# Kernel optimization log

Hardware: AMD Instinct MI355X
Metric: run time of the kernel (lower is better)

Reference implementation:

```python
import jax, jax.numpy as jnp
import numpy as np

N = 50000
F_IN = 512
H = 256
L = 52
E = 1600000


def gcn_conv(x, W, b, src, dst):
    """PyG GCNConv: add self-loops, symmetric norm D^-1/2 (A+I) D^-1/2, then X W + b.
    src/dst already include self-loops."""
    h = x @ W  # [N, H]
    deg = jax.ops.segment_sum(jnp.ones_like(dst, dtype=h.dtype), dst, num_segments=N)
    dinv = jnp.where(deg > 0, jax.lax.rsqrt(deg), 0.0)
    w = dinv[src] * dinv[dst]  # [E+N]
    out = jax.ops.segment_sum(h[src] * w[:, None], dst, num_segments=N)
    return out + b


def _branch(x, src, dst, params):
    (W1, b1), (W2, b2), (W3, b3), (We, be) = params
    x = jax.nn.relu(gcn_conv(x, W1, b1, src, dst))
    x = jax.nn.relu(gcn_conv(x, W2, b2, src, dst))
    x = jax.nn.relu(gcn_conv(x, W3, b3, src, dst))
    return gcn_conv(x, We, be, src, dst)


def setup_inputs() -> dict:
    key = jax.random.key(0)
    ks = jax.random.split(key, 32)
    d = {}
    d["x_1"] = jax.random.normal(ks[0], (N, F_IN), dtype=jnp.float32)
    d["x_2"] = jax.random.normal(ks[1], (N, F_IN), dtype=jnp.float32)
    d["edge_index_1"] = jax.random.randint(ks[2], (2, E), 0, N, dtype=jnp.int32)
    d["edge_index_2"] = jax.random.randint(ks[3], (2, E), 0, N, dtype=jnp.int32)

    def lin(k, fi, fo):
        s = 1.0 / np.sqrt(fi)
        return jax.random.uniform(k, (fi, fo), jnp.float32, -s, s)

    i = 4
    for br in (1, 2):
        fis = [F_IN, H, H, H]
        for li, nm in enumerate(["1", "2", "3", "e"]):
            d[f"Wc{nm}{br}"] = lin(ks[i], fis[li], H); i += 1
            d[f"bc{nm}{br}"] = jnp.zeros((H,), jnp.float32)
    d["w1_W"] = lin(ks[i], H, 1); i += 1
    d["w1_b"] = jnp.zeros((1,), jnp.float32)
    d["w2_W"] = lin(ks[i], H, 1); i += 1
    d["w2_b"] = jnp.zeros((1,), jnp.float32)
    d["fin_W"] = lin(ks[i], H, H); i += 1
    d["fin_b"] = jnp.zeros((H,), jnp.float32)
    d["out_W"] = lin(ks[i], H, L); i += 1
    d["out_b"] = jnp.zeros((L,), jnp.float32)
    return d


def reference(x_1, edge_index_1, x_2, edge_index_2,
              Wc11, bc11, Wc21, bc21, Wc31, bc31, Wce1, bce1,
              Wc12, bc12, Wc22, bc22, Wc32, bc32, Wce2, bce2,
              w1_W, w1_b, w2_W, w2_b, fin_W, fin_b, out_W, out_b):
    loop = jnp.arange(N)
    s1 = jnp.concatenate([edge_index_1[0], loop])
    d1 = jnp.concatenate([edge_index_1[1], loop])
    s2 = jnp.concatenate([edge_index_2[0], loop])
    d2 = jnp.concatenate([edge_index_2[1], loop])

    h1 = _branch(x_1, s1, d1, [(Wc11, bc11), (Wc21, bc21), (Wc31, bc31), (Wce1, bce1)])
    h2 = _branch(x_2, s2, d2, [(Wc12, bc12), (Wc22, bc22), (Wc32, bc32), (Wce2, bce2)])

    f1 = jax.nn.sigmoid(h1 @ w1_W + w1_b)  # [N,1]
    f2 = jax.nn.sigmoid(h2 @ w2_W + w2_b)
    f1 = f1 / (f1 + f2)
    out = f1 * h1 + (1.0 - f1) * h2
    out = jax.nn.relu(out @ fin_W + fin_b)
    return jax.nn.sigmoid(out @ out_W + out_b)
```

## Files before the change

### kernel.cpp

```cpp
#include <hip/hip_runtime.h>
#include <math.h>

#define N_NODES 50000
#define F_IN    512
#define HDIM    256
#define L_OUT   52
#define E_EDGES 1600000
#define NB1     391
#define EB      2048
#define NBLK    782

typedef short short8 __attribute__((ext_vector_type(8)));
typedef unsigned short u16x8 __attribute__((ext_vector_type(8)));
typedef float f32x4 __attribute__((ext_vector_type(4)));
typedef float f32x2 __attribute__((ext_vector_type(2)));

__device__ __forceinline__ float bf2f(unsigned short u) {
    unsigned int x = ((unsigned int)u) << 16;
    return __builtin_bit_cast(float, x);
}
__device__ __forceinline__ unsigned short f2bf(float f) {
    unsigned int u = __builtin_bit_cast(unsigned int, f);
    return (unsigned short)((u + 0x7fffu + ((u >> 16) & 1u)) >> 16);
}
__device__ __forceinline__ unsigned char f2fp8(float f) {
    int pk = __builtin_amdgcn_cvt_pk_fp8_f32(f, 0.f, 0, false);
    return (unsigned char)(pk & 0xff);
}
__device__ __forceinline__ void gload16(const unsigned short* g, unsigned short* l) {
    __builtin_amdgcn_global_load_lds(
        (const __attribute__((address_space(1))) unsigned int*)(g),
        (__attribute__((address_space(3))) unsigned int*)(l), 16, 0, 0);
}


__global__ __launch_bounds__(256) void k_hist(const int* __restrict__ d1, const int* __restrict__ d2,
                                              int* __restrict__ h1, int* __restrict__ h2, int E) {
    const int* D = blockIdx.y ? d2 : d1;
    int* H = blockIdx.y ? h2 : h1;
    __shared__ int h[NB1];
    for (int t = threadIdx.x; t < NB1; t += 256) h[t] = 0;
    __syncthreads();
    int base = blockIdx.x * EB;
#pragma unroll
    for (int k = 0; k < 8; k++) {
        int e = base + k * 256 + threadIdx.x;
        if (e < E) atomicAdd(&h[D[e] >> 7], 1);
    }
    __syncthreads();
    for (int t = threadIdx.x; t < NB1; t += 256)
        H[(size_t)t * NBLK + blockIdx.x] = h[t];
}

__global__ __launch_bounds__(256) void k_scanb(int* __restrict__ h1, int* __restrict__ h2,
                                               int* __restrict__ t1, int* __restrict__ t2) {
    int* H = blockIdx.y ? h2 : h1;
    int* T = blockIdx.y ? t2 : t1;
    int b = blockIdx.x;
    __shared__ int s[256];
    int carry = 0;
    for (int base = 0; base < NBLK; base += 256) {
        int i = base + threadIdx.x;
        int v = (i < NBLK) ? H[(size_t)b * NBLK + i] : 0;
        s[threadIdx.x] = v;
        __syncthreads();
        for (int off = 1; off < 256; off <<= 1) {
            int t = (threadIdx.x >= off) ? s[threadIdx.x - off] : 0;
            __syncthreads();
            s[threadIdx.x] += t;
            __syncthreads();
        }
        if (i < NBLK) H[(size_t)b * NBLK + i] = carry + s[threadIdx.x] - v;
        int ct = s[255];
        __syncthreads();
        carry += ct;
    }
    if (threadIdx.x == 0) T[b] = carry;
}

__global__ __launch_bounds__(512) void k_bstart(const int* __restrict__ t1, const int* __restrict__ t2,
                                                int* __restrict__ b1, int* __restrict__ b2,
                                                int* __restrict__ rp1, int* __restrict__ rp2,
                                                int N, int E) {
    const int* T = blockIdx.y ? t2 : t1;
    int* BS = blockIdx.y ? b2 : b1;
    int* RP = blockIdx.y ? rp2 : rp1;
    __shared__ int s[512];
    int v = (threadIdx.x < NB1) ? T[threadIdx.x] : 0;
    s[threadIdx.x] = v;
    __syncthreads();
    for (int off = 1; off < 512; off <<= 1) {
        int t = (threadIdx.x >= off) ? s[threadIdx.x - off] : 0;
        __syncthreads();
        s[threadIdx.x] += t;
        __syncthreads();
    }
    if (threadIdx.x < NB1) BS[threadIdx.x] = s[threadIdx.x] - v;
    if (threadIdx.x == 0) { BS[NB1] = E; RP[N] = E; }
}

__global__ __launch_bounds__(256) void k_scatter(const int* __restrict__ s1, const int* __restrict__ d1,
                                                 const int* __restrict__ s2, const int* __restrict__ d2,
                                                 const int* __restrict__ h1, const int* __restrict__ h2,
                                                 const int* __restrict__ b1, const int* __restrict__ b2,
                                                 unsigned int* __restrict__ r1, unsigned int* __restrict__ r2,
                                                 int E) {
    int br = blockIdx.y;
    const int* S = br ? s2 : s1;
    const int* D = br ? d2 : d1;
    const int* H = br ? h2 : h1;
    const int* BS = br ? b2 : b1;
    unsigned int* R = br ? r2 : r1;
    __shared__ int cur[NB1];
    for (int t = threadIdx.x; t < NB1; t += 256)
        cur[t] = BS[t] + H[(size_t)t * NBLK + blockIdx.x];
    __syncthreads();
    int base = blockIdx.x * EB;
#pragma unroll
    for (int k = 0; k < 8; k++) {
        int e = base + k * 256 + threadIdx.x;
        if (e < E) {
            int d = D[e];
            int p = atomicAdd(&cur[d >> 7], 1);
            R[p] = (unsigned int)(S[e] & 0xFFFF) | ((unsigned int)d << 16);
        }
    }
}

__global__ __launch_bounds__(256) void k_sort(const unsigned int* __restrict__ r1,
                                              const unsigned int* __restrict__ r2,
                                              const int* __restrict__ b1, const int* __restrict__ b2,
                                              int* __restrict__ c1, int* __restrict__ c2,
                                              int* __restrict__ rp1, int* __restrict__ rp2,
                                              unsigned short* __restrict__ col1,
                                              unsigned short* __restrict__ col2, int N) {
    int br = blockIdx.y;
    const unsigned int* R = br ? r2 : r1;
    const int* BS = br ? b2 : b1;
    int* CNT = br ? c2 : c1;
    int* RP = br ? rp2 : rp1;
    unsigned short* COL = br ? col2 : col1;
    int b = blockIdx.x;
    int s = BS[b], sz = BS[b + 1] - s;
    __shared__ int h[128], sc[128], cur[128];
    if (threadIdx.x < 128) h[threadIdx.x] = 0;
    __syncthreads();
    for (int i = s + threadIdx.x; i < s + sz; i += 256)
        atomicAdd(&h[(R[i] >> 16) & 127], 1);
    __syncthreads();
    if (threadIdx.x < 128) sc[threadIdx.x] = h[threadIdx.x];
    __syncthreads();
    for (int off = 1; off < 128; off <<= 1) {
        int t = 0;
        if (threadIdx.x < 128 && threadIdx.x >= off) t = sc[threadIdx.x - off];
        __syncthreads();
        if (threadIdx.x < 128) sc[threadIdx.x] += t;
        __syncthreads();
    }
    if (threadIdx.x < 128) {
        int excl = sc[threadIdx.x] - h[threadIdx.x];
        cur[threadIdx.x] = excl;
        int node = b * 128 + threadIdx.x;
        if (node < N) { CNT[node] = h[threadIdx.x]; RP[node] = s + excl; }
    }
    __syncthreads();
    for (int i = s + threadIdx.x; i < s + sz; i += 256) {
        unsigned int r = R[i];
        int low = (r >> 16) & 127;
        int p = atomicAdd(&cur[low], 1);
        COL[s + p] = (unsigned short)(r & 0xFFFFu);
    }
}


__global__ void k_dinv2(const int* __restrict__ c1, const int* __restrict__ c2,
                        float* __restrict__ v1, float* __restrict__ v2, int n) {
    int i = blockIdx.x * blockDim.x + threadIdx.x;
    if (i < n) v1[i] = rsqrtf((float)(c1[i] + 1));
    else if (i < 2 * n) v2[i - n] = rsqrtf((float)(c2[i - n] + 1));
}

__global__ void k_f2b2(const float* __restrict__ x1, const float* __restrict__ x2,
                       unsigned short* __restrict__ o1, unsigned short* __restrict__ o2,
                       int n4) {
    int i = blockIdx.x * blockDim.x + threadIdx.x;
    int stride = gridDim.x * blockDim.x;
    int tot = 2 * n4;
    for (; i < tot; i += stride) {
        int br = i >= n4;
        int e = br ? i - n4 : i;
        float4 v = ((const float4*)(br ? x2 : x1))[e];
        ushort4 o;
        o.x = f2bf(v.x); o.y = f2bf(v.y); o.z = f2bf(v.z); o.w = f2bf(v.w);
        ((ushort4*)(br ? o2 : o1))[e] = o;
    }
}

struct WDesc { const float* in; unsigned short* out; int K; int N; int Npad; };
struct WPack { WDesc d[10]; };

__global__ void k_wconv(WPack p) {
    WDesc w = p.d[blockIdx.y];
    int total = w.K * w.Npad;
    int idx = blockIdx.x * 256 + threadIdx.x;
    if (idx >= total) return;
    int n = idx / w.K, k = idx - n * w.K;
    w.out[idx] = (n < w.N) ? f2bf(w.in[(size_t)k * w.N + n]) : (unsigned short)0;
}


__global__ void k_agg(const unsigned char* __restrict__ g, const int* __restrict__ rowptr,
                      const unsigned short* __restrict__ col,
                      const float* __restrict__ dinv,
                      const float* __restrict__ bias, unsigned short* __restrict__ out,
                      int n, int do_relu) {
    int gtid = blockIdx.x * blockDim.x + threadIdx.x;
    int wid = gtid >> 6;
    if (wid >= n) return;
    int lane = threadIdx.x & 63;
    int half = lane >> 5;
    int fl = lane & 31;

    float di = dinv[wid];

    float a[8];
#pragma unroll
    for (int k = 0; k < 8; k++) a[k] = 0.f;

    int r0 = rowptr[wid], r1 = rowptr[wid + 1];
    int base = r0;

    for (; base + 32 <= r1; base += 32) {
        int c[16]; float w[16]; uint2 v[16];
#pragma unroll
        for (int t = 0; t < 16; t++) c[t] = col[base + 2 * t + half];
#pragma unroll
        for (int t = 0; t < 16; t++) w[t] = dinv[c[t]];
#pragma unroll
        for (int t = 0; t < 16; t++)
            v[t] = ((const uint2*)(g + (size_t)c[t] * HDIM))[fl];
#pragma unroll
        for (int t = 0; t < 16; t++) {
            float wt = w[t] * di;
            f32x2 p0 = __builtin_amdgcn_cvt_pk_f32_fp8((int)v[t].x, false);
            f32x2 p1 = __builtin_amdgcn_cvt_pk_f32_fp8((int)v[t].x, true);
            f32x2 p2 = __builtin_amdgcn_cvt_pk_f32_fp8((int)v[t].y, false);
            f32x2 p3 = __builtin_amdgcn_cvt_pk_f32_fp8((int)v[t].y, true);
            a[0] = fmaf(p0[0], wt, a[0]); a[1] = fmaf(p0[1], wt, a[1]);
            a[2] = fmaf(p1[0], wt, a[2]); a[3] = fmaf(p1[1], wt, a[3]);
            a[4] = fmaf(p2[0], wt, a[4]); a[5] = fmaf(p2[1], wt, a[5]);
            a[6] = fmaf(p3[0], wt, a[6]); a[7] = fmaf(p3[1], wt, a[7]);
        }
    }
    for (; base + 16 <= r1; base += 16) {
        int c[8]; float w[8]; uint2 v[8];
#pragma unroll
        for (int t = 0; t < 8; t++) c[t] = col[base + 2 * t + half];
#pragma unroll
        for (int t = 0; t < 8; t++) w[t] = dinv[c[t]];
#pragma unroll
        for (int t = 0; t < 8; t++)
            v[t] = ((const uint2*)(g + (size_t)c[t] * HDIM))[fl];
#pragma unroll
        for (int t = 0; t < 8; t++) {
            float wt = w[t] * di;
            f32x2 p0 = __builtin_amdgcn_cvt_pk_f32_fp8((int)v[t].x, false);
            f32x2 p1 = __builtin_amdgcn_cvt_pk_f32_fp8((int)v[t].x, true);
            f32x2 p2 = __builtin_amdgcn_cvt_pk_f32_fp8((int)v[t].y, false);
            f32x2 p3 = __builtin_amdgcn_cvt_pk_f32_fp8((int)v[t].y, true);
            a[0] = fmaf(p0[0], wt, a[0]); a[1] = fmaf(p0[1], wt, a[1]);
            a[2] = fmaf(p1[0], wt, a[2]); a[3] = fmaf(p1[1], wt, a[3]);
            a[4] = fmaf(p2[0], wt, a[4]); a[5] = fmaf(p2[1], wt, a[5]);
            a[6] = fmaf(p3[0], wt, a[6]); a[7] = fmaf(p3[1], wt, a[7]);
        }
    }
    if (base < r1) {
        int c[8]; float w[8]; uint2 v[8];
#pragma unroll
        for (int t = 0; t < 8; t++) {
            int idx = base + 2 * t + half;
            int ok = idx < r1;
            c[t] = col[ok ? idx : r0];
            w[t] = ok ? dinv[c[t]] : 0.f;
        }
#pragma unroll
        for (int t = 0; t < 8; t++)
            v[t] = ((const uint2*)(g + (size_t)c[t] * HDIM))[fl];
#pragma unroll
        for (int t = 0; t < 8; t++) {
            float wt = w[t] * di;
            f32x2 p0 = __builtin_amdgcn_cvt_pk_f32_fp8((int)v[t].x, false);
            f32x2 p1 = __builtin_amdgcn_cvt_pk_f32_fp8((int)v[t].x, true);
            f32x2 p2 = __builtin_amdgcn_cvt_pk_f32_fp8((int)v[t].y, false);
            f32x2 p3 = __builtin_amdgcn_cvt_pk_f32_fp8((int)v[t].y, true);
            a[0] = fmaf(p0[0], wt, a[0]); a[1] = fmaf(p0[1], wt, a[1]);
            a[2] = fmaf(p1[0], wt, a[2]); a[3] = fmaf(p1[1], wt, a[3]);
            a[4] = fmaf(p2[0], wt, a[4]); a[5] = fmaf(p2[1], wt, a[5]);
            a[6] = fmaf(p3[0], wt, a[6]); a[7] = fmaf(p3[1], wt, a[7]);
        }
    }

#pragma unroll
    for (int k = 0; k < 8; k++) a[k] += __shfl_xor(a[k], 32);

    float w0 = di * di;
    uint2 sv = ((const uint2*)(g + (size_t)wid * HDIM))[fl];
    f32x2 s0 = __builtin_amdgcn_cvt_pk_f32_fp8((int)sv.x, false);
    f32x2 s1 = __builtin_amdgcn_cvt_pk_f32_fp8((int)sv.x, true);
    f32x2 s2 = __builtin_amdgcn_cvt_pk_f32_fp8((int)sv.y, false);
    f32x2 s3 = __builtin_amdgcn_cvt_pk_f32_fp8((int)sv.y, true);
    float sf[8] = {s0[0], s0[1], s1[0], s1[1], s2[0], s2[1], s3[0], s3[1]};
    u16x8 o;
#pragma unroll
    for (int k = 0; k < 8; k++) {
        float x = fmaf(sf[k], w0, a[k]) + bias[fl * 8 + k];
        if (do_relu) x = fmaxf(x, 0.f);
        o[k] = f2bf(x);
    }
    if (half == 0)
        ((u16x8*)(out + (size_t)wid * HDIM))[fl] = o;
}


template <int EPI>
__global__ __launch_bounds__(256) void k_gemm(const unsigned short* __restrict__ A,
                                              const unsigned short* __restrict__ Bt,
                                              const float* __restrict__ bias,
                                              void* __restrict__ Cout,
                                              int M, int K, int Nc) {
    __shared__ __align__(16) unsigned short As[128 * 32];
    __shared__ __align__(16) unsigned short Bs[128 * 32];
    int tid = threadIdx.x;
    int wid = tid >> 6, lane = tid & 63;
    int wr = wid >> 1, wc = wid & 1;
    int mb = blockIdx.y * 128, nb = blockIdx.x * 128;

    int sr = tid >> 2;
    int ssl = (tid & 3) ^ ((sr >> 1) & 3);
    int ar0 = mb + sr;      if (ar0 > M - 1) ar0 = M - 1;
    int ar1 = mb + sr + 64; if (ar1 > M - 1) ar1 = M - 1;
    const unsigned short* gA0 = A + (size_t)ar0 * K + ssl * 8;
    const unsigned short* gA1 = A + (size_t)ar1 * K + ssl * 8;
    const unsigned short* gB0 = Bt + (size_t)(nb + sr) * K + ssl * 8;
    const unsigned short* gB1 = Bt + (size_t)(nb + sr + 64) * K + ssl * 8;
    unsigned short* ldsA = As + tid * 8;
    unsigned short* ldsB = Bs + tid * 8;

    f32x4 acc[4][4];
#pragma unroll
    for (int m = 0; m < 4; m++)
#pragma unroll
        for (int n = 0; n < 4; n++) acc[m][n] = (f32x4){0.f, 0.f, 0.f, 0.f};

    int l15 = lane & 15, ks = lane >> 4;

    for (int k0 = 0; k0 < K; k0 += 32) {
        gload16(gA0 + k0, ldsA);
        gload16(gA1 + k0, ldsA + 2048);
        gload16(gB0 + k0, ldsB);
        gload16(gB1 + k0, ldsB + 2048);
        __syncthreads();

        short8 af[4], bfr[4];
#pragma unroll
        for (int m = 0; m < 4; m++) {
            int row = wr * 64 + m * 16 + l15;
            int slot = ks ^ ((row >> 1) & 3);
            af[m] = *(const short8*)((const char*)As + row * 64 + slot * 16);
        }
#pragma unroll
        for (int n = 0; n < 4; n++) {
            int row = wc * 64 + n * 16 + l15;
            int slot = ks ^ ((row >> 1) & 3);
            bfr[n] = *(const short8*)((const char*)Bs + row * 64 + slot * 16);
        }
#pragma unroll
        for (int m = 0; m < 4; m++)
#pragma unroll
            for (int n = 0; n < 4; n++)
                acc[m][n] = __builtin_amdgcn_mfma_f32_16x16x32_bf16(af[m], bfr[n], acc[m][n], 0, 0, 0);
        __syncthreads();
    }

    int lq = lane >> 4;
#pragma unroll
    for (int m = 0; m < 4; m++) {
#pragma unroll
        for (int n = 0; n < 4; n++) {
            int gcol = nb + wc * 64 + n * 16 + l15;
#pragma unroll
            for (int r = 0; r < 4; r++) {
                int grow = mb + wr * 64 + m * 16 + lq * 4 + r;
                if (grow >= M) continue;
                float v = acc[m][n][r];
                if (EPI == 0) {
                    ((unsigned char*)Cout)[(size_t)grow * Nc + gcol] = f2fp8(v);
                } else if (EPI == 1) {
                    v += bias[gcol];
                    v = fmaxf(v, 0.f);
                    ((unsigned short*)Cout)[(size_t)grow * Nc + gcol] = f2bf(v);
                } else {
                    if (gcol < Nc) {
                        v += bias[gcol];
                        v = 1.f / (1.f + expf(-v));
                        ((float*)Cout)[(size_t)grow * Nc + gcol] = v;
                    }
                }
            }
        }
    }
}


__global__ void k_gate(const unsigned short* __restrict__ h1, const unsigned short* __restrict__ h2,
                       const float* __restrict__ w1, const float* __restrict__ w1b,
                       const float* __restrict__ w2, const float* __restrict__ w2b,
                       unsigned short* __restrict__ m, int n) {
    int gtid = blockIdx.x * blockDim.x + threadIdx.x;
    int wid = gtid >> 6;
    int lane = threadIdx.x & 63;
    if (wid >= n) return;
    ushort4 av = ((const ushort4*)(h1 + (size_t)wid * HDIM))[lane];
    ushort4 bv = ((const ushort4*)(h2 + (size_t)wid * HDIM))[lane];
    float4 wa = ((const float4*)w1)[lane];
    float4 wb = ((const float4*)w2)[lane];
    float a0 = bf2f(av.x), a1 = bf2f(av.y), a2 = bf2f(av.z), a3 = bf2f(av.w);
    float b0 = bf2f(bv.x), b1 = bf2f(bv.y), b2 = bf2f(bv.z), b3 = bf2f(bv.w);
    float d1 = a0 * wa.x + a1 * wa.y + a2 * wa.z + a3 * wa.w;
    float d2 = b0 * wb.x + b1 * wb.y + b2 * wb.z + b3 * wb.w;
    for (int off = 32; off > 0; off >>= 1) {
        d1 += __shfl_xor(d1, off);
        d2 += __shfl_xor(d2, off);
    }
    float f1 = 1.f / (1.f + expf(-(d1 + w1b[0])));
    float f2 = 1.f / (1.f + expf(-(d2 + w2b[0])));
    float f = f1 / (f1 + f2);
    ushort4 o;
    o.x = f2bf(f * a0 + (1.f - f) * b0);
    o.y = f2bf(f * a1 + (1.f - f) * b1);
    o.z = f2bf(f * a2 + (1.f - f) * b2);
    o.w = f2bf(f * a3 + (1.f - f) * b3);
    ((ushort4*)(m + (size_t)wid * HDIM))[lane] = o;
}


extern "C" void kernel_launch(void* const* d_in, const int* in_sizes, int n_in,
                              void* d_out, int out_size, void* d_ws, size_t ws_size,
                              hipStream_t stream) {
    (void)n_in; (void)out_size; (void)ws_size;
    const int N = N_NODES, E = E_EDGES;

    const float* x1; const float* x2; const int* ei1; const int* ei2;
    if (in_sizes[1] == 2 * E) {
        x1 = (const float*)d_in[0]; ei1 = (const int*)d_in[1];
        x2 = (const float*)d_in[2]; ei2 = (const int*)d_in[3];
    } else {
        x1 = (const float*)d_in[0]; x2 = (const float*)d_in[1];
        ei1 = (const int*)d_in[2]; ei2 = (const int*)d_in[3];
    }
    const float* W[2][4]; const float* Bv[2][4];
    int idx = 4;
    for (int br = 0; br < 2; br++)
        for (int l = 0; l < 4; l++) {
            W[br][l] = (const float*)d_in[idx++];
            Bv[br][l] = (const float*)d_in[idx++];
        }
    const float* w1W  = (const float*)d_in[20];
    const float* w1b  = (const float*)d_in[21];
    const float* w2W  = (const float*)d_in[22];
    const float* w2b  = (const float*)d_in[23];
    const float* finW = (const float*)d_in[24];
    const float* finb = (const float*)d_in[25];
    const float* outW = (const float*)d_in[26];
    const float* outb = (const float*)d_in[27];
    float* out = (float*)d_out;

    size_t off = 0;
    auto alloc = [&](size_t bytes) {
        void* p = (char*)d_ws + off;
        off = (off + bytes + 255) & ~(size_t)255;
        return p;
    };
    unsigned short* x1b = (unsigned short*)alloc((size_t)N * F_IN * 2);
    unsigned short* x2b = (unsigned short*)alloc((size_t)N * F_IN * 2);
    unsigned char*  g8  = (unsigned char*)alloc((size_t)N * HDIM);
    unsigned short* mb_ = (unsigned short*)alloc((size_t)N * HDIM * 2);
    unsigned short* h1b = (unsigned short*)alloc((size_t)N * HDIM * 2);
    unsigned short* h2b = (unsigned short*)alloc((size_t)N * HDIM * 2);
    unsigned short* Wt[2][4];
    Wt[0][0] = (unsigned short*)alloc((size_t)HDIM * F_IN * 2);
    for (int l = 1; l < 4; l++) Wt[0][l] = (unsigned short*)alloc((size_t)HDIM * HDIM * 2);
    Wt[1][0] = (unsigned short*)alloc((size_t)HDIM * F_IN * 2);
    for (int l = 1; l < 4; l++) Wt[1][l] = (unsigned short*)alloc((size_t)HDIM * HDIM * 2);
    unsigned short* finWt = (unsigned short*)alloc((size_t)HDIM * HDIM * 2);
    unsigned short* outWt = (unsigned short*)alloc((size_t)128 * HDIM * 2);
    unsigned short* col1 = (unsigned short*)alloc((size_t)E * 2);
    unsigned short* col2 = (unsigned short*)alloc((size_t)E * 2);
    unsigned int* rec1 = (unsigned int*)alloc((size_t)E * 4);
    unsigned int* rec2 = (unsigned int*)alloc((size_t)E * 4);
    int* hist1  = (int*)alloc((size_t)NB1 * NBLK * 4);
    int* hist2  = (int*)alloc((size_t)NB1 * NBLK * 4);
    int* tot1   = (int*)alloc((size_t)NB1 * 4);
    int* tot2   = (int*)alloc((size_t)NB1 * 4);
    int* bs1    = (int*)alloc((size_t)(NB1 + 1) * 4);
    int* bs2    = (int*)alloc((size_t)(NB1 + 1) * 4);
    int* rp1    = (int*)alloc((size_t)(N + 1) * 4);
    int* rp2    = (int*)alloc((size_t)(N + 1) * 4);
    int* cnt1   = (int*)alloc((size_t)N * 4);
    int* cnt2   = (int*)alloc((size_t)N * 4);
    float* di1  = (float*)alloc((size_t)N * 4);
    float* di2  = (float*)alloc((size_t)N * 4);

    const int BLK = 256;
    int nwaves_grid = (N * 64 + BLK - 1) / BLK;
    int mtiles = (N + 127) / 128;
    dim3 grid_h(HDIM / 128, mtiles);
    dim3 grid_o(1, mtiles);

    WPack wp;
    wp.d[0] = {W[0][0], Wt[0][0], F_IN, HDIM, HDIM};
    wp.d[1] = {W[0][1], Wt[0][1], HDIM, HDIM, HDIM};
    wp.d[2] = {W[0][2], Wt[0][2], HDIM, HDIM, HDIM};
    wp.d[3] = {W[0][3], Wt[0][3], HDIM, HDIM, HDIM};
    wp.d[4] = {W[1][0], Wt[1][0], F_IN, HDIM, HDIM};
    wp.d[5] = {W[1][1], Wt[1][1], HDIM, HDIM, HDIM};
    wp.d[6] = {W[1][2], Wt[1][2], HDIM, HDIM, HDIM};
    wp.d[7] = {W[1][3], Wt[1][3], HDIM, HDIM, HDIM};
    wp.d[8] = {finW, finWt, HDIM, HDIM, HDIM};
    wp.d[9] = {outW, outWt, HDIM, L_OUT, 128};
    k_wconv<<<dim3(512, 10), BLK, 0, stream>>>(wp);
    k_f2b2<<<4096, BLK, 0, stream>>>(x1, x2, x1b, x2b, N * F_IN / 4);

    k_hist<<<dim3(NBLK, 2), BLK, 0, stream>>>(ei1 + E, ei2 + E, hist1, hist2, E);
    k_scanb<<<dim3(NB1, 2), BLK, 0, stream>>>(hist1, hist2, tot1, tot2);
    k_bstart<<<dim3(1, 2), 512, 0, stream>>>(tot1, tot2, bs1, bs2, rp1, rp2, N, E);
    k_scatter<<<dim3(NBLK, 2), BLK, 0, stream>>>(ei1, ei1 + E, ei2, ei2 + E,
                                                 hist1, hist2, bs1, bs2, rec1, rec2, E);
    k_sort<<<dim3(NB1, 2), BLK, 0, stream>>>(rec1, rec2, bs1, bs2,
                                             cnt1, cnt2, rp1, rp2, col1, col2, N);
    k_dinv2<<<(2 * N + BLK - 1) / BLK, BLK, 0, stream>>>(cnt1, cnt2, di1, di2, N);

    for (int br = 0; br < 2; br++) {
        const unsigned short* col = br ? col2 : col1;
        const int* rp = br ? rp2 : rp1;
        const float* di = br ? di2 : di1;
        const unsigned short* xb = br ? x2b : x1b;
        unsigned short* hb = br ? h2b : h1b;

        k_gemm<0><<<grid_h, BLK, 0, stream>>>(xb, Wt[br][0], nullptr, g8, N, F_IN, HDIM);
        k_agg<<<nwaves_grid, BLK, 0, stream>>>(g8, rp, col, di, Bv[br][0], hb, N, 1);
        for (int l = 1; l <= 2; l++) {
            k_gemm<0><<<grid_h, BLK, 0, stream>>>(hb, Wt[br][l], nullptr, g8, N, HDIM, HDIM);
            k_agg<<<nwaves_grid, BLK, 0, stream>>>(g8, rp, col, di, Bv[br][l], hb, N, 1);
        }
        k_gemm<0><<<grid_h, BLK, 0, stream>>>(hb, Wt[br][3], nullptr, g8, N, HDIM, HDIM);
        k_agg<<<nwaves_grid, BLK, 0, stream>>>(g8, rp, col, di, Bv[br][3], hb, N, 0);
    }

    k_gate<<<nwaves_grid, BLK, 0, stream>>>(h1b, h2b, w1W, w1b, w2W, w2b, mb_, N);
    k_gemm<1><<<grid_h, BLK, 0, stream>>>(mb_, finWt, finb, x1b, N, HDIM, HDIM);
    k_gemm<2><<<grid_o, BLK, 0, stream>>>(x1b, outWt, outb, out, N, HDIM, L_OUT);
}
```

Before: 892.6 us.

## Fuse fp32-to-bf16 input conversion into first GEMM and widen aggregation loads

Removes the standalone kernel that converted both fp32 node-feature matrices to bf16. The first-layer GEMM now reads fp32 rows directly and converts them to bf16 in registers before storing to LDS, which saves a full write-and-reread of the converted input. Separately, the aggregation kernel now has each lane load 16 fp8 values (uint4) instead of 8, so each wave handles four edges at a time with a two-step shuffle reduction. The trade-offs are losing the asynchronous global-to-LDS load path for the A operand in that GEMM, doubling fp32 A-read traffic there, and higher register pressure in the aggregation kernel.

```diff
diff --git a/kernel.cpp b/kernel.cpp
--- a/kernel.cpp
+++ b/kernel.cpp
@@ -26,6 +26,11 @@
 __device__ __forceinline__ unsigned char f2fp8(float f) {
     int pk = __builtin_amdgcn_cvt_pk_fp8_f32(f, 0.f, 0, false);
     return (unsigned char)(pk & 0xff);
+}
+__device__ __forceinline__ void fp8x4_to_f32(unsigned int u, float* f) {
+    f32x2 p0 = __builtin_amdgcn_cvt_pk_f32_fp8((int)u, false);
+    f32x2 p1 = __builtin_amdgcn_cvt_pk_f32_fp8((int)u, true);
+    f[0] = p0[0]; f[1] = p0[1]; f[2] = p1[0]; f[3] = p1[1];
 }
 __device__ __forceinline__ void gload16(const unsigned short* g, unsigned short* l) {
     __builtin_amdgcn_global_load_lds(
@@ -180,22 +185,6 @@
     else if (i < 2 * n) v2[i - n] = rsqrtf((float)(c2[i - n] + 1));
 }
 
-__global__ void k_f2b2(const float* __restrict__ x1, const float* __restrict__ x2,
-                       unsigned short* __restrict__ o1, unsigned short* __restrict__ o2,
-                       int n4) {
-    int i = blockIdx.x * blockDim.x + threadIdx.x;
-    int stride = gridDim.x * blockDim.x;
-    int tot = 2 * n4;
-    for (; i < tot; i += stride) {
-        int br = i >= n4;
-        int e = br ? i - n4 : i;
-        float4 v = ((const float4*)(br ? x2 : x1))[e];
-        ushort4 o;
-        o.x = f2bf(v.x); o.y = f2bf(v.y); o.z = f2bf(v.z); o.w = f2bf(v.w);
-        ((ushort4*)(br ? o2 : o1))[e] = o;
-    }
-}
-
 struct WDesc { const float* in; unsigned short* out; int K; int N; int Npad; };
 struct WPack { WDesc d[10]; };
 
@@ -218,112 +207,116 @@
     int wid = gtid >> 6;
     if (wid >= n) return;
     int lane = threadIdx.x & 63;
-    int half = lane >> 5;
-    int fl = lane & 31;
+    int q = lane >> 4;
+    int fl = lane & 15;
 
     float di = dinv[wid];
 
-    float a[8];
-#pragma unroll
-    for (int k = 0; k < 8; k++) a[k] = 0.f;
+    float a[16];
+#pragma unroll
+    for (int k = 0; k < 16; k++) a[k] = 0.f;
 
     int r0 = rowptr[wid], r1 = rowptr[wid + 1];
     int base = r0;
 
     for (; base + 32 <= r1; base += 32) {
-        int c[16]; float w[16]; uint2 v[16];
-#pragma unroll
-        for (int t = 0; t < 16; t++) c[t] = col[base + 2 * t + half];
-#pragma unroll
-        for (int t = 0; t < 16; t++) w[t] = dinv[c[t]];
-#pragma unroll
-        for (int t = 0; t < 16; t++)
-            v[t] = ((const uint2*)(g + (size_t)c[t] * HDIM))[fl];
-#pragma unroll
-        for (int t = 0; t < 16; t++) {
-            float wt = w[t] * di;
-            f32x2 p0 = __builtin_amdgcn_cvt_pk_f32_fp8((int)v[t].x, false);
-            f32x2 p1 = __builtin_amdgcn_cvt_pk_f32_fp8((int)v[t].x, true);
-            f32x2 p2 = __builtin_amdgcn_cvt_pk_f32_fp8((int)v[t].y, false);
-            f32x2 p3 = __builtin_amdgcn_cvt_pk_f32_fp8((int)v[t].y, true);
-            a[0] = fmaf(p0[0], wt, a[0]); a[1] = fmaf(p0[1], wt, a[1]);
-            a[2] = fmaf(p1[0], wt, a[2]); a[3] = fmaf(p1[1], wt, a[3]);
-            a[4] = fmaf(p2[0], wt, a[4]); a[5] = fmaf(p2[1], wt, a[5]);
-            a[6] = fmaf(p3[0], wt, a[6]); a[7] = fmaf(p3[1], wt, a[7]);
-        }
-    }
-    for (; base + 16 <= r1; base += 16) {
-        int c[8]; float w[8]; uint2 v[8];
-#pragma unroll
-        for (int t = 0; t < 8; t++) c[t] = col[base + 2 * t + half];
+        int c[8]; float w[8]; uint4 v[8];
+#pragma unroll
+        for (int t = 0; t < 8; t++) c[t] = col[base + 4 * t + q];
 #pragma unroll
         for (int t = 0; t < 8; t++) w[t] = dinv[c[t]];
 #pragma unroll
         for (int t = 0; t < 8; t++)
-            v[t] = ((const uint2*)(g + (size_t)c[t] * HDIM))[fl];
+            v[t] = ((const uint4*)(g + (size_t)c[t] * HDIM))[fl];
 #pragma unroll
         for (int t = 0; t < 8; t++) {
             float wt = w[t] * di;
-            f32x2 p0 = __builtin_amdgcn_cvt_pk_f32_fp8((int)v[t].x, false);
-            f32x2 p1 = __builtin_amdgcn_cvt_pk_f32_fp8((int)v[t].x, true);
-            f32x2 p2 = __builtin_amdgcn_cvt_pk_f32_fp8((int)v[t].y, false);
-            f32x2 p3 = __builtin_amdgcn_cvt_pk_f32_fp8((int)v[t].y, true);
-            a[0] = fmaf(p0[0], wt, a[0]); a[1] = fmaf(p0[1], wt, a[1]);
-            a[2] = fmaf(p1[0], wt, a[2]); a[3] = fmaf(p1[1], wt, a[3]);
-            a[4] = fmaf(p2[0], wt, a[4]); a[5] = fmaf(p2[1], wt, a[5]);
-            a[6] = fmaf(p3[0], wt, a[6]); a[7] = fmaf(p3[1], wt, a[7]);
+            float f[16];
+            fp8x4_to_f32(v[t].x, f);
+            fp8x4_to_f32(v[t].y, f + 4);
+            fp8x4_to_f32(v[t].z, f + 8);
+            fp8x4_to_f32(v[t].w, f + 12);
+#pragma unroll
+            for (int k = 0; k < 16; k++) a[k] = fmaf(f[k], wt, a[k]);
+        }
+    }
+    for (; base + 16 <= r1; base += 16) {
+        int c[4]; float w[4]; uint4 v[4];
+#pragma unroll
+        for (int t = 0; t < 4; t++) c[t] = col[base + 4 * t + q];
+#pragma unroll
+        for (int t = 0; t < 4; t++) w[t] = dinv[c[t]];
+#pragma unroll
+        for (int t = 0; t < 4; t++)
+            v[t] = ((const uint4*)(g + (size_t)c[t] * HDIM))[fl];
+#pragma unroll
+        for (int t = 0; t < 4; t++) {
+            float wt = w[t] * di;
+            float f[16];
+            fp8x4_to_f32(v[t].x, f);
+            fp8x4_to_f32(v[t].y, f + 4);
+            fp8x4_to_f32(v[t].z, f + 8);
+            fp8x4_to_f32(v[t].w, f + 12);
+#pragma unroll
+            for (int k = 0; k < 16; k++) a[k] = fmaf(f[k], wt, a[k]);
         }
     }
     if (base < r1) {
-        int c[8]; float w[8]; uint2 v[8];
-#pragma unroll
-        for (int t = 0; t < 8; t++) {
-            int idx = base + 2 * t + half;
+        int c[4]; float w[4]; uint4 v[4];
+#pragma unroll
+        for (int t = 0; t < 4; t++) {
+            int idx = base + 4 * t + q;
             int ok = idx < r1;
             c[t] = col[ok ? idx : r0];
             w[t] = ok ? dinv[c[t]] : 0.f;
         }
 #pragma unroll
-        for (int t = 0; t < 8; t++)
-            v[t] = ((const uint2*)(g + (size_t)c[t] * HDIM))[fl];
-#pragma unroll
-        for (int t = 0; t < 8; t++) {
+        for (int t = 0; t < 4; t++)
+            v[t] = ((const uint4*)(g + (size_t)c[t] * HDIM))[fl];
+#pragma unroll
+        for (int t = 0; t < 4; t++) {
             float wt = w[t] * di;
-            f32x2 p0 = __builtin_amdgcn_cvt_pk_f32_fp8((int)v[t].x, false);
-            f32x2 p1 = __builtin_amdgcn_cvt_pk_f32_fp8((int)v[t].x, true);
-            f32x2 p2 = __builtin_amdgcn_cvt_pk_f32_fp8((int)v[t].y, false);
-            f32x2 p3 = __builtin_amdgcn_cvt_pk_f32_fp8((int)v[t].y, true);
-            a[0] = fmaf(p0[0], wt, a[0]); a[1] = fmaf(p0[1], wt, a[1]);
-            a[2] = fmaf(p1[0], wt, a[2]); a[3] = fmaf(p1[1], wt, a[3]);
-            a[4] = fmaf(p2[0], wt, a[4]); a[5] = fmaf(p2[1], wt, a[5]);
-            a[6] = fmaf(p3[0], wt, a[6]); a[7] = fmaf(p3[1], wt, a[7]);
-        }
-    }
-
-#pragma unroll
-    for (int k = 0; k < 8; k++) a[k] += __shfl_xor(a[k], 32);
+            float f[16];
+            fp8x4_to_f32(v[t].x, f);
+            fp8x4_to_f32(v[t].y, f + 4);
+            fp8x4_to_f32(v[t].z, f + 8);
+            fp8x4_to_f32(v[t].w, f + 12);
+#pragma unroll
+            for (int k = 0; k < 16; k++) a[k] = fmaf(f[k], wt, a[k]);
+        }
+    }
+
+#pragma unroll
+    for (int k = 0; k < 16; k++) {
+        a[k] += __shfl_xor(a[k], 16);
+        a[k] += __shfl_xor(a[k], 32);
+    }
 
     float w0 = di * di;
-    uint2 sv = ((const uint2*)(g + (size_t)wid * HDIM))[fl];
-    f32x2 s0 = __builtin_amdgcn_cvt_pk_f32_fp8((int)sv.x, false);
-    f32x2 s1 = __builtin_amdgcn_cvt_pk_f32_fp8((int)sv.x, true);
-    f32x2 s2 = __builtin_amdgcn_cvt_pk_f32_fp8((int)sv.y, false);
-    f32x2 s3 = __builtin_amdgcn_cvt_pk_f32_fp8((int)sv.y, true);
-    float sf[8] = {s0[0], s0[1], s1[0], s1[1], s2[0], s2[1], s3[0], s3[1]};
-    u16x8 o;
-#pragma unroll
-    for (int k = 0; k < 8; k++) {
-        float x = fmaf(sf[k], w0, a[k]) + bias[fl * 8 + k];
+    uint4 sv = ((const uint4*)(g + (size_t)wid * HDIM))[fl];
+    float sf[16];
+    fp8x4_to_f32(sv.x, sf); fp8x4_to_f32(sv.y, sf + 4);
+    fp8x4_to_f32(sv.z, sf + 8); fp8x4_to_f32(sv.w, sf + 12);
+    const float4* b4 = (const float4*)(bias + fl * 16);
+    float4 bb0 = b4[0], bb1 = b4[1], bb2 = b4[2], bb3 = b4[3];
+    float bf_[16] = {bb0.x, bb0.y, bb0.z, bb0.w, bb1.x, bb1.y, bb1.z, bb1.w,
+                     bb2.x, bb2.y, bb2.z, bb2.w, bb3.x, bb3.y, bb3.z, bb3.w};
+    u16x8 o0, o1;
+#pragma unroll
+    for (int k = 0; k < 16; k++) {
+        float x = fmaf(sf[k], w0, a[k]) + bf_[k];
         if (do_relu) x = fmaxf(x, 0.f);
-        o[k] = f2bf(x);
-    }
-    if (half == 0)
-        ((u16x8*)(out + (size_t)wid * HDIM))[fl] = o;
-}
-
-
-template <int EPI>
-__global__ __launch_bounds__(256) void k_gemm(const unsigned short* __restrict__ A,
+        if (k < 8) o0[k] = f2bf(x); else o1[k - 8] = f2bf(x);
+    }
+    if (q == 0) {
+        u16x8* dst = (u16x8*)(out + (size_t)wid * HDIM + fl * 16);
+        dst[0] = o0; dst[1] = o1;
+    }
+}
+
+
+template <int EPI, int AF32>
+__global__ __launch_bounds__(256) void k_gemm(const void* __restrict__ Ain,
                                               const unsigned short* __restrict__ Bt,
                                               const float* __restrict__ bias,
                                               void* __restrict__ Cout,
@@ -339,8 +332,12 @@
     int ssl = (tid & 3) ^ ((sr >> 1) & 3);
     int ar0 = mb + sr;      if (ar0 > M - 1) ar0 = M - 1;
     int ar1 = mb + sr + 64; if (ar1 > M - 1) ar1 = M - 1;
-    const unsigned short* gA0 = A + (size_t)ar0 * K + ssl * 8;
-    const unsigned short* gA1 = A + (size_t)ar1 * K + ssl * 8;
+    const unsigned short* A16 = (const unsigned short*)Ain;
+    const float* A32 = (const float*)Ain;
+    const unsigned short* gA0 = A16 + (size_t)ar0 * K + ssl * 8;
+    const unsigned short* gA1 = A16 + (size_t)ar1 * K + ssl * 8;
+    const float* fA0 = A32 + (size_t)ar0 * K + ssl * 8;
+    const float* fA1 = A32 + (size_t)ar1 * K + ssl * 8;
     const unsigned short* gB0 = Bt + (size_t)(nb + sr) * K + ssl * 8;
     const unsigned short* gB1 = Bt + (size_t)(nb + sr + 64) * K + ssl * 8;
     unsigned short* ldsA = As + tid * 8;
@@ -355,8 +352,22 @@
     int l15 = lane & 15, ks = lane >> 4;
 
     for (int k0 = 0; k0 < K; k0 += 32) {
-        gload16(gA0 + k0, ldsA);
-        gload16(gA1 + k0, ldsA + 2048);
+        if (AF32) {
+            float4 a0 = ((const float4*)(fA0 + k0))[0];
+            float4 a1 = ((const float4*)(fA0 + k0))[1];
+            float4 b0 = ((const float4*)(fA1 + k0))[0];
+            float4 b1 = ((const float4*)(fA1 + k0))[1];
+            u16x8 w0, w1;
+            w0[0] = f2bf(a0.x); w0[1] = f2bf(a0.y); w0[2] = f2bf(a0.z); w0[3] = f2bf(a0.w);
+            w0[4] = f2bf(a1.x); w0[5] = f2bf(a1.y); w0[6] = f2bf(a1.z); w0[7] = f2bf(a1.w);
+            w1[0] = f2bf(b0.x); w1[1] = f2bf(b0.y); w1[2] = f2bf(b0.z); w1[3] = f2bf(b0.w);
+            w1[4] = f2bf(b1.x); w1[5] = f2bf(b1.y); w1[6] = f2bf(b1.z); w1[7] = f2bf(b1.w);
+            *(u16x8*)ldsA = w0;
+            *(u16x8*)(ldsA + 2048) = w1;
+        } else {
+            gload16(gA0 + k0, ldsA);
+            gload16(gA1 + k0, ldsA + 2048);
+        }
         gload16(gB0 + k0, ldsB);
         gload16(gB1 + k0, ldsB + 2048);
         __syncthreads();
@@ -481,10 +492,9 @@
         off = (off + bytes + 255) & ~(size_t)255;
         return p;
     };
-    unsigned short* x1b = (unsigned short*)alloc((size_t)N * F_IN * 2);
-    unsigned short* x2b = (unsigned short*)alloc((size_t)N * F_IN * 2);
     unsigned char*  g8  = (unsigned char*)alloc((size_t)N * HDIM);
     unsigned short* mb_ = (unsigned short*)alloc((size_t)N * HDIM * 2);
+    unsigned short* tb_ = (unsigned short*)alloc((size_t)N * HDIM * 2);
     unsigned short* h1b = (unsigned short*)alloc((size_t)N * HDIM * 2);
     unsigned short* h2b = (unsigned short*)alloc((size_t)N * HDIM * 2);
     unsigned short* Wt[2][4];
@@ -529,7 +539,6 @@
     wp.d[8] = {finW, finWt, HDIM, HDIM, HDIM};
     wp.d[9] = {outW, outWt, HDIM, L_OUT, 128};
     k_wconv<<<dim3(512, 10), BLK, 0, stream>>>(wp);
-    k_f2b2<<<4096, BLK, 0, stream>>>(x1, x2, x1b, x2b, N * F_IN / 4);
 
     k_hist<<<dim3(NBLK, 2), BLK, 0, stream>>>(ei1 + E, ei2 + E, hist1, hist2, E);
     k_scanb<<<dim3(NB1, 2), BLK, 0, stream>>>(hist1, hist2, tot1, tot2);
@@ -544,20 +553,20 @@
         const unsigned short* col = br ? col2 : col1;
         const int* rp = br ? rp2 : rp1;
         const float* di = br ? di2 : di1;
-        const unsigned short* xb = br ? x2b : x1b;
+        const float* x = br ? x2 : x1;
         unsigned short* hb = br ? h2b : h1b;
 
-        k_gemm<0><<<grid_h, BLK, 0, stream>>>(xb, Wt[br][0], nullptr, g8, N, F_IN, HDIM);
+        k_gemm<0, 1><<<grid_h, BLK, 0, stream>>>(x, Wt[br][0], nullptr, g8, N, F_IN, HDIM);
         k_agg<<<nwaves_grid, BLK, 0, stream>>>(g8, rp, col, di, Bv[br][0], hb, N, 1);
         for (int l = 1; l <= 2; l++) {
-            k_gemm<0><<<grid_h, BLK, 0, stream>>>(hb, Wt[br][l], nullptr, g8, N, HDIM, HDIM);
+            k_gemm<0, 0><<<grid_h, BLK, 0, stream>>>(hb, Wt[br][l], nullptr, g8, N, HDIM, HDIM);
             k_agg<<<nwaves_grid, BLK, 0, stream>>>(g8, rp, col, di, Bv[br][l], hb, N, 1);
         }
-        k_gemm<0><<<grid_h, BLK, 0, stream>>>(hb, Wt[br][3], nullptr, g8, N, HDIM, HDIM);
+        k_gemm<0, 0><<<grid_h, BLK, 0, stream>>>(hb, Wt[br][3], nullptr, g8, N, HDIM, HDIM);
         k_agg<<<nwaves_grid, BLK, 0, stream>>>(g8, rp, col, di, Bv[br][3], hb, N, 0);
     }
 
     k_gate<<<nwaves_grid, BLK, 0, stream>>>(h1b, h2b, w1W, w1b, w2W, w2b, mb_, N);
-    k_gemm<1><<<grid_h, BLK, 0, stream>>>(mb_, finWt, finb, x1b, N, HDIM, HDIM);
-    k_gemm<2><<<grid_o, BLK, 0, stream>>>(x1b, outWt, outb, out, N, HDIM, L_OUT);
-}
+    k_gemm<1, 0><<<grid_h, BLK, 0, stream>>>(mb_, finWt, finb, tb_, N, HDIM, HDIM);
+    k_gemm<2, 0><<<grid_o, BLK, 0, stream>>>(tb_, outWt, outb, out, N, HDIM, L_OUT);
+}
```

After: 957.5 us. 1.07x slower.
